# Optimization experiments

Hardware: AMD Instinct MI355X
Metric: run time of the kernel (lower is better)

Reference implementation:

```python
import jax, jax.numpy as jnp
import numpy as np

N_NODES = 200000
N_EDGES = 600000
EMB = 128
HID = 128
N_RELS = 64
N_MOTIFS = 512
N_CENTERS = 256
N_NODE_CLASSES = 16


def _linear_params(key, out_dim, in_dim):
    kw, kb = jax.random.split(key)
    s = 1.0 / np.sqrt(in_dim)
    w = jax.random.uniform(kw, (out_dim, in_dim), jnp.float32, -s, s)
    b = jax.random.uniform(kb, (out_dim,), jnp.float32, -s, s)
    return w, b


def setup_inputs() -> dict:
    key = jax.random.key(0)
    ks = jax.random.split(key, 12)
    lin_w, lin_b = _linear_params(ks[2], HID, EMB)
    conv1_w, conv1_b = _linear_params(ks[3], HID, HID)
    conv2_w, conv2_b = _linear_params(ks[4], HID, HID)
    edge_w, edge_b = _linear_params(ks[5], N_RELS, 2 * HID)
    motif_w, motif_b = _linear_params(ks[6], N_MOTIFS, HID)
    node_w, node_b = _linear_params(ks[7], N_NODE_CLASSES, HID)
    return {
        "node_emb": jax.random.normal(ks[0], (N_NODES, EMB), jnp.float32),
        "rel_emb": jax.random.normal(ks[1], (N_RELS, EMB), jnp.float32),
        "lin_w": lin_w, "lin_b": lin_b,
        "conv1_w": conv1_w, "conv1_b": conv1_b,
        "conv2_w": conv2_w, "conv2_b": conv2_b,
        "edge_w": edge_w, "edge_b": edge_b,
        "motif_w": motif_w, "motif_b": motif_b,
        "node_w": node_w, "node_b": node_b,
        "node_ids": jnp.arange(N_NODES, dtype=jnp.int32),
        "rel_ids": jax.random.randint(ks[8], (N_EDGES,), 0, N_RELS, jnp.int32),
        "center_mol_idx": jax.random.randint(ks[9], (N_CENTERS,), 0, N_NODES, jnp.int32),
        "edge_index": jax.random.randint(ks[10], (2, N_EDGES), 0, N_NODES, jnp.int32),
    }


def _gine_conv(x, edge_index, edge_attr, w, b):
    # PyG GINEConv (eps=0): nn((1+eps)*x + sum_j relu(x_j + e_ji))
    src, dst = edge_index[0], edge_index[1]
    msg = jax.nn.relu(x[src] + edge_attr)               # [E, H]
    agg = jax.ops.segment_sum(msg, dst, num_segments=x.shape[0])  # [N, H]
    return (agg + x) @ w.T + b


def reference(node_emb, rel_emb, lin_w, lin_b, conv1_w, conv1_b,
              conv2_w, conv2_b, edge_w, edge_b, motif_w, motif_b,
              node_w, node_b, node_ids, rel_ids, center_mol_idx, edge_index):
    x = node_emb[node_ids]            # [N, EMB]
    edge_attr = rel_emb[rel_ids]      # [E, EMB]
    x = x @ lin_w.T + lin_b           # [N, H]
    edge_attr = edge_attr @ lin_w.T + lin_b  # [E, H]
    x = _gine_conv(x, edge_index, edge_attr, conv1_w, conv1_b)
    x = jax.nn.relu(x)
    x = _gine_conv(x, edge_index, edge_attr, conv2_w, conv2_b)
    edge_pred_input = jnp.concatenate([x[edge_index[0]], x[edge_index[1]]], axis=1)  # [E, 2H]
    edge_class = edge_pred_input @ edge_w.T + edge_b       # [E, num_rels]
    center = x[center_mol_idx]                             # [C, H]
    motif_pred = center @ motif_w.T + motif_b              # [C, num_motifs]
    node_class = x @ node_w.T + node_b                     # [N, 16]
    return (edge_class, motif_pred, node_class)
```

## Files before the change

kernel.cpp:

```cpp
#include <hip/hip_runtime.h>
#include <hip/hip_bf16.h>

#define N_NODES 200000
#define N_EDGES 600000
#define EMB 128
#define HID 128
#define N_RELS 64
#define N_MOTIFS 512
#define N_CENTERS 256
#define NCLS 16

#define SCAN_C 512
#define NB_SCAN ((N_NODES + SCAN_C - 1) / SCAN_C)

typedef unsigned short u16;
typedef __attribute__((ext_vector_type(8))) short short8;
typedef __attribute__((ext_vector_type(4))) float f32x4;

__device__ __forceinline__ float bf2f(u16 u) {
    unsigned int i = ((unsigned int)u) << 16;
    float f; __builtin_memcpy(&f, &i, 4); return f;
}
__device__ __forceinline__ u16 f2bf(float f) {
    unsigned int x; __builtin_memcpy(&x, &f, 4);
    x += 0x7fffu + ((x >> 16) & 1u);
    return (u16)(x >> 16);
}

#define O_LINW   0
#define O_LINB   16384
#define O_C1W    16512
#define O_C1B    32896
#define O_C2W    33024
#define O_C2B    49408
#define O_EW     49536
#define O_EB     65920
#define O_MW     65984
#define O_MB     131520
#define O_NW     132032
#define O_NB     134080
#define N_WB     134096

__global__ void k_pre(const float* __restrict__ rel_emb,
                      const float* __restrict__ lw, const float* __restrict__ lb,
                      const float* __restrict__ c1w, const float* __restrict__ c1b,
                      const float* __restrict__ c2w, const float* __restrict__ c2b,
                      const float* __restrict__ ew, const float* __restrict__ eb,
                      const float* __restrict__ mw, const float* __restrict__ mb,
                      const float* __restrict__ nw, const float* __restrict__ nb,
                      float* __restrict__ rel_lin, u16* __restrict__ rel_bf,
                      u16* __restrict__ wb)
{
    if (blockIdx.x < 64) {
        __shared__ float e[EMB];
        const int r = blockIdx.x, h = threadIdx.x;
        e[h] = rel_emb[r * EMB + h];
        __syncthreads();
        const float* wr = lw + (size_t)h * EMB;
        float acc = lb[h];
        #pragma unroll
        for (int k0 = 0; k0 < EMB; k0 += 4) {
            f32x4 wv = *(const f32x4*)(wr + k0);
            #pragma unroll
            for (int j = 0; j < 4; ++j) acc += e[k0 + j] * wv[j];
        }
        rel_lin[r * HID + h] = acc;
        rel_bf[r * HID + h] = f2bf(acc);
        return;
    }
    const int t = (blockIdx.x - 64) * 128 + threadIdx.x;
    if (t >= N_WB) return;
    float v;
    if      (t < O_LINB) v = lw[t - O_LINW];
    else if (t < O_C1W)  v = lb[t - O_LINB];
    else if (t < O_C1B)  v = c1w[t - O_C1W];
    else if (t < O_C2W)  v = c1b[t - O_C1B];
    else if (t < O_C2B)  v = c2w[t - O_C2W];
    else if (t < O_EW)   v = c2b[t - O_C2B];
    else if (t < O_EB)   v = ew[t - O_EW];
    else if (t < O_MW)   v = eb[t - O_EB];
    else if (t < O_MB)   v = mw[t - O_MW];
    else if (t < O_NW)   v = mb[t - O_MB];
    else if (t < O_NB)   v = nw[t - O_NW];
    else                 v = nb[t - O_NB];
    wb[t] = f2bf(v);
}

__global__ void k_hist(const int* __restrict__ dst, int* __restrict__ deg)
{
    const int e = blockIdx.x * 256 + threadIdx.x;
    if (e < N_EDGES) atomicAdd(&deg[dst[e]], 1);
}

__global__ void k_scan1(const int* __restrict__ deg, int* __restrict__ bsum)
{
    __shared__ int sd[256];
    const int t = threadIdx.x, base = blockIdx.x * SCAN_C;
    int v = 0;
    int i0 = base + t, i1 = base + 256 + t;
    if (i0 < N_NODES) v += deg[i0];
    if (i1 < N_NODES) v += deg[i1];
    sd[t] = v; __syncthreads();
    for (int s = 128; s > 0; s >>= 1) {
        if (t < s) sd[t] += sd[t + s];
        __syncthreads();
    }
    if (t == 0) bsum[blockIdx.x] = sd[0];
}

__global__ void k_scan2(int* __restrict__ bsum, int* __restrict__ row_ptr)
{
    __shared__ int sh[512];
    const int t = threadIdx.x;
    int v = (t < NB_SCAN) ? bsum[t] : 0;
    sh[t] = v;
    for (int off = 1; off < 512; off <<= 1) {
        __syncthreads();
        int a = (t >= off) ? sh[t - off] : 0;
        __syncthreads();
        sh[t] += a;
    }
    __syncthreads();
    if (t < NB_SCAN) bsum[t] = sh[t] - v;
    if (t == 511) row_ptr[N_NODES] = sh[511];
}

__global__ void k_scan3(const int* __restrict__ deg, const int* __restrict__ bsum,
                        int* __restrict__ row_ptr)
{
    __shared__ int sh[256];
    const int t = threadIdx.x, base = blockIdx.x * SCAN_C;
    const int i0 = base + 2 * t, i1 = i0 + 1;
    int d0 = (i0 < N_NODES) ? deg[i0] : 0;
    int d1 = (i1 < N_NODES) ? deg[i1] : 0;
    int p = d0 + d1;
    sh[t] = p;
    for (int off = 1; off < 256; off <<= 1) {
        __syncthreads();
        int a = (t >= off) ? sh[t - off] : 0;
        __syncthreads();
        sh[t] += a;
    }
    __syncthreads();
    const int off = bsum[blockIdx.x] + sh[t] - p;
    if (i0 < N_NODES) row_ptr[i0] = off;
    if (i1 < N_NODES) row_ptr[i1] = off + d0;
}

__global__ void k_fill(const int* __restrict__ src, const int* __restrict__ dst,
                       const int* __restrict__ rid, const int* __restrict__ row_ptr,
                       int* __restrict__ cur, int* __restrict__ srcrid)
{
    const int e = blockIdx.x * 256 + threadIdx.x;
    if (e >= N_EDGES) return;
    const int d = dst[e];
    const int pos = row_ptr[d] + atomicAdd(&cur[d], 1);
    srcrid[pos] = src[e] * 64 + rid[e];
}

__global__ __launch_bounds__(256) void k_lin(
    const float* __restrict__ emb, const int* __restrict__ ids,
    const u16* __restrict__ w, const u16* __restrict__ bias,
    u16* __restrict__ out)
{
    const int wid = threadIdx.x >> 6, lane = threadIdx.x & 63;
    const int r15 = lane & 15, kg = (lane >> 4) * 8;
    const int arow = blockIdx.x * 64 + wid * 16 + r15;
    const int srow = ids[arow];
    const float* ar = emb + (size_t)srow * EMB + kg;
    short8 a[4];
    #pragma unroll
    for (int kk = 0; kk < 4; ++kk) {
        f32x4 a0 = *(const f32x4*)(ar + kk * 32);
        f32x4 a1 = *(const f32x4*)(ar + kk * 32 + 4);
        short8 t;
        #pragma unroll
        for (int j = 0; j < 4; ++j) { t[j] = (short)f2bf(a0[j]); t[4 + j] = (short)f2bf(a1[j]); }
        a[kk] = t;
    }
    f32x4 acc[8];
    #pragma unroll
    for (int nb = 0; nb < 8; ++nb) acc[nb] = (f32x4){0.f, 0.f, 0.f, 0.f};
    #pragma unroll
    for (int nb = 0; nb < 8; ++nb) {
        const u16* wr = w + (size_t)(nb * 16 + r15) * EMB + kg;
        #pragma unroll
        for (int kk = 0; kk < 4; ++kk) {
            short8 bv = *(const short8*)(wr + kk * 32);
            acc[nb] = __builtin_amdgcn_mfma_f32_16x16x32_bf16(a[kk], bv, acc[nb], 0, 0, 0);
        }
    }
    const int ob = blockIdx.x * 64 + wid * 16 + (lane >> 4) * 4;
    #pragma unroll
    for (int nb = 0; nb < 8; ++nb) {
        const int col = nb * 16 + r15;
        const float bn = bf2f(bias[col]);
        #pragma unroll
        for (int r = 0; r < 4; ++r)
            out[(size_t)(ob + r) * HID + col] = f2bf(acc[nb][r] + bn);
    }
}

__global__ __launch_bounds__(256) void k_msg2(
    const u16* __restrict__ x, const u16* __restrict__ relb,
    const int* __restrict__ srcrid, u16* __restrict__ msg)
{
    const int t = blockIdx.x * 256 + threadIdx.x;
    const int p = t >> 2;
    const int q = (t & 3) * 32;
    const int v = srcrid[p];
    const int s = v >> 6, r = v & 63;
    const u16* xp = x + (size_t)s * HID + q;
    const u16* rp = relb + r * HID + q;
    u16* mp = msg + (size_t)p * HID + q;
    #pragma unroll
    for (int c = 0; c < 4; ++c) {
        short8 xv = *(const short8*)(xp + c * 8);
        short8 rv = *(const short8*)(rp + c * 8);
        short8 o;
        #pragma unroll
        for (int j = 0; j < 8; ++j)
            o[j] = (short)f2bf(fmaxf(bf2f((u16)xv[j]) + bf2f((u16)rv[j]), 0.f));
        *(short8*)(mp + c * 8) = o;
    }
}

__global__ __launch_bounds__(256) void k_fuse2(
    const u16* __restrict__ x, const u16* __restrict__ msg,
    const int* __restrict__ row_ptr,
    const u16* __restrict__ w, const u16* __restrict__ bias,
    u16* __restrict__ out, const int do_relu)
{
    const int wid = threadIdx.x >> 6, lane = threadIdx.x & 63;
    const int r15 = lane & 15;
    const int kg = (lane >> 4) * 8;
    const int n = blockIdx.x * 64 + wid * 16 + r15;
    const int pbeg = row_ptr[n], pend = row_ptr[n + 1];

    float acc[32];
    #pragma unroll
    for (int j = 0; j < 32; ++j) acc[j] = 0.f;

    int p = pbeg;
    for (; p + 2 <= pend; p += 2) {
        const u16* m0 = msg + (size_t)p * HID + kg;
        const u16* m1 = m0 + HID;
        short8 v0[4], v1[4];
        #pragma unroll
        for (int kk = 0; kk < 4; ++kk) { v0[kk] = *(const short8*)(m0 + kk * 32);
                                         v1[kk] = *(const short8*)(m1 + kk * 32); }
        #pragma unroll
        for (int kk = 0; kk < 4; ++kk)
            #pragma unroll
            for (int j = 0; j < 8; ++j)
                acc[kk * 8 + j] += bf2f((u16)v0[kk][j]) + bf2f((u16)v1[kk][j]);
    }
    if (p < pend) {
        const u16* m0 = msg + (size_t)p * HID + kg;
        #pragma unroll
        for (int kk = 0; kk < 4; ++kk) {
            short8 v0 = *(const short8*)(m0 + kk * 32);
            #pragma unroll
            for (int j = 0; j < 8; ++j) acc[kk * 8 + j] += bf2f((u16)v0[j]);
        }
    }

    short8 a[4];
    {
        const u16* xp = x + (size_t)n * HID + kg;
        #pragma unroll
        for (int kk = 0; kk < 4; ++kk) {
            short8 xv = *(const short8*)(xp + kk * 32);
            short8 t;
            #pragma unroll
            for (int j = 0; j < 8; ++j) t[j] = (short)f2bf(acc[kk * 8 + j] + bf2f((u16)xv[j]));
            a[kk] = t;
        }
    }

    f32x4 accm[8];
    #pragma unroll
    for (int nb = 0; nb < 8; ++nb) accm[nb] = (f32x4){0.f, 0.f, 0.f, 0.f};
    #pragma unroll
    for (int nb = 0; nb < 8; ++nb) {
        const u16* wr = w + (size_t)(nb * 16 + r15) * HID + kg;
        #pragma unroll
        for (int kk = 0; kk < 4; ++kk) {
            short8 bv = *(const short8*)(wr + kk * 32);
            accm[nb] = __builtin_amdgcn_mfma_f32_16x16x32_bf16(a[kk], bv, accm[nb], 0, 0, 0);
        }
    }
    const int ob = blockIdx.x * 64 + wid * 16 + (lane >> 4) * 4;
    #pragma unroll
    for (int nb = 0; nb < 8; ++nb) {
        const int col = nb * 16 + r15;
        const float bn = bf2f(bias[col]);
        #pragma unroll
        for (int r = 0; r < 4; ++r) {
            float v = accm[nb][r] + bn;
            if (do_relu) v = fmaxf(v, 0.f);
            out[(size_t)(ob + r) * HID + col] = f2bf(v);
        }
    }
}

__global__ __launch_bounds__(256) void k_heads(
    const u16* __restrict__ x2, const u16* __restrict__ ew,
    const u16* __restrict__ nw, const u16* __restrict__ nbias,
    u16* __restrict__ y, float* __restrict__ node_out)
{
    const int wid = threadIdx.x >> 6, lane = threadIdx.x & 63;
    const int r15 = lane & 15, kg = (lane >> 4) * 8;
    const int arow = blockIdx.x * 64 + wid * 16 + r15;
    const u16* xr = x2 + (size_t)arow * HID + kg;
    short8 a[4];
    #pragma unroll
    for (int kk = 0; kk < 4; ++kk) a[kk] = *(const short8*)(xr + kk * 32);

    f32x4 accs[4], accd[4], accn;
    #pragma unroll
    for (int nb = 0; nb < 4; ++nb) {
        accs[nb] = (f32x4){0.f, 0.f, 0.f, 0.f};
        accd[nb] = (f32x4){0.f, 0.f, 0.f, 0.f};
    }
    accn = (f32x4){0.f, 0.f, 0.f, 0.f};

    #pragma unroll
    for (int nb = 0; nb < 4; ++nb) {
        const u16* wr = ew + (size_t)(nb * 16 + r15) * 256 + kg;
        #pragma unroll
        for (int kk = 0; kk < 4; ++kk) {
            short8 bs = *(const short8*)(wr + kk * 32);
            short8 bd = *(const short8*)(wr + 128 + kk * 32);
            accs[nb] = __builtin_amdgcn_mfma_f32_16x16x32_bf16(a[kk], bs, accs[nb], 0, 0, 0);
            accd[nb] = __builtin_amdgcn_mfma_f32_16x16x32_bf16(a[kk], bd, accd[nb], 0, 0, 0);
        }
    }
    {
        const u16* wr = nw + (size_t)r15 * HID + kg;
        #pragma unroll
        for (int kk = 0; kk < 4; ++kk) {
            short8 bv = *(const short8*)(wr + kk * 32);
            accn = __builtin_amdgcn_mfma_f32_16x16x32_bf16(a[kk], bv, accn, 0, 0, 0);
        }
    }

    const int ob = blockIdx.x * 64 + wid * 16 + (lane >> 4) * 4;
    #pragma unroll
    for (int nb = 0; nb < 4; ++nb) {
        const int col = nb * 16 + r15;
        #pragma unroll
        for (int r = 0; r < 4; ++r) {
            y[(size_t)(ob + r) * 128 + col] = f2bf(accs[nb][r]);
            y[(size_t)(ob + r) * 128 + 64 + col] = f2bf(accd[nb][r]);
        }
    }
    const float bn = bf2f(nbias[r15]);
    #pragma unroll
    for (int r = 0; r < 4; ++r)
        node_out[(size_t)(ob + r) * NCLS + r15] = accn[r] + bn;
}

__global__ __launch_bounds__(256) void k_eout(
    const u16* __restrict__ y, const int* __restrict__ src, const int* __restrict__ dst,
    const float* __restrict__ eb, float* __restrict__ out)
{
    const int t = blockIdx.x * 256 + threadIdx.x;
    const int e = t >> 2;
    const int qq = (t & 3) * 16;
    const int s = src[e], d = dst[e];
    const u16* ys = y + (size_t)s * 128 + qq;
    const u16* yd = y + (size_t)d * 128 + 64 + qq;
    const float* ebp = eb + qq;
    float* op = out + (size_t)e * 64 + qq;
    #pragma unroll
    for (int c = 0; c < 2; ++c) {
        short8 vs = *(const short8*)(ys + c * 8);
        short8 vd = *(const short8*)(yd + c * 8);
        #pragma unroll
        for (int h = 0; h < 2; ++h) {
            f32x4 vb = *(const f32x4*)(ebp + c * 8 + h * 4);
            f32x4 r;
            #pragma unroll
            for (int j = 0; j < 4; ++j)
                r[j] = bf2f((u16)vs[h * 4 + j]) + bf2f((u16)vd[h * 4 + j]) + vb[j];
            *(f32x4*)(op + c * 8 + h * 4) = r;
        }
    }
}

__global__ void k_motif(const u16* __restrict__ x2, const int* __restrict__ centers,
                        const u16* __restrict__ mw, const u16* __restrict__ mb,
                        float* __restrict__ out)
{
    __shared__ float xs[HID];
    const int c = blockIdx.x, m = threadIdx.x;
    if (m < HID) xs[m] = bf2f(x2[(size_t)centers[c] * HID + m]);
    __syncthreads();
    const u16* wr = mw + (size_t)m * HID;
    float acc = bf2f(mb[m]);
    #pragma unroll
    for (int k0 = 0; k0 < HID; k0 += 8) {
        short8 wv = *(const short8*)(wr + k0);
        #pragma unroll
        for (int j = 0; j < 8; ++j) acc += xs[k0 + j] * bf2f((u16)wv[j]);
    }
    out[(size_t)c * N_MOTIFS + m] = acc;
}

extern "C" void kernel_launch(void* const* d_in, const int* in_sizes, int n_in,
                              void* d_out, int out_size, void* d_ws, size_t ws_size,
                              hipStream_t stream)
{
    const float* node_emb = (const float*)d_in[0];
    const float* rel_emb  = (const float*)d_in[1];
    const float* lin_w    = (const float*)d_in[2];
    const float* lin_b    = (const float*)d_in[3];
    const float* conv1_w  = (const float*)d_in[4];
    const float* conv1_b  = (const float*)d_in[5];
    const float* conv2_w  = (const float*)d_in[6];
    const float* conv2_b  = (const float*)d_in[7];
    const float* edge_w   = (const float*)d_in[8];
    const float* edge_b   = (const float*)d_in[9];
    const float* motif_w  = (const float*)d_in[10];
    const float* motif_b  = (const float*)d_in[11];
    const float* node_w   = (const float*)d_in[12];
    const float* node_b   = (const float*)d_in[13];
    const int* node_ids = (const int*)d_in[14];
    const int* rel_ids  = (const int*)d_in[15];
    const int* centers  = (const int*)d_in[16];
    const int* src      = (const int*)d_in[17];
    const int* dst      = ((const int*)d_in[17]) + N_EDGES;

    char* ws = (char*)d_ws;
    float* rel_lin = (float*)ws;
    u16*   wb      = (u16*)(ws + 32768);
    u16*   rel_bf  = (u16*)(ws + 393216);
    u16*   x0      = (u16*)(ws + 524288);
    u16*   x1      = (u16*)(ws + 524288 + 51200000);
    u16*   y       = (u16*)(ws + 524288 + 2 * 51200000);
    char*  csr     = ws + 524288 + 3 * 51200000;
    int*   deg     = (int*)csr;
    int*   cur     = (int*)(csr + 800000);
    int*   row_ptr = (int*)(csr + 1600000);
    int*   srcrid  = (int*)(csr + 2400032);
    int*   bsum    = (int*)(csr + 4800032);
    u16*   x2      = x0;

    float* out_edge  = (float*)d_out;
    float* out_motif = out_edge + (size_t)N_EDGES * 64;
    float* out_node  = out_motif + (size_t)N_CENTERS * N_MOTIFS;

    u16* msg = (u16*)d_out;

    k_pre<<<64 + (N_WB + 127) / 128, 128, 0, stream>>>(
        rel_emb, lin_w, lin_b, conv1_w, conv1_b, conv2_w, conv2_b,
        edge_w, edge_b, motif_w, motif_b, node_w, node_b, rel_lin, rel_bf, wb);
    hipMemsetAsync(deg, 0, 1600000, stream);

    k_hist<<<(N_EDGES + 255) / 256, 256, 0, stream>>>(dst, deg);
    k_scan1<<<NB_SCAN, 256, 0, stream>>>(deg, bsum);
    k_scan2<<<1, 512, 0, stream>>>(bsum, row_ptr);
    k_scan3<<<NB_SCAN, 256, 0, stream>>>(deg, bsum, row_ptr);
    k_fill<<<(N_EDGES + 255) / 256, 256, 0, stream>>>(src, dst, rel_ids, row_ptr, cur, srcrid);

    k_lin<<<N_NODES / 64, 256, 0, stream>>>(node_emb, node_ids, wb + O_LINW, wb + O_LINB, x0);

    k_msg2<<<(N_EDGES * 4) / 256, 256, 0, stream>>>(x0, rel_bf, srcrid, msg);
    k_fuse2<<<N_NODES / 64, 256, 0, stream>>>(x0, msg, row_ptr,
                                              wb + O_C1W, wb + O_C1B, x1, 1);
    k_msg2<<<(N_EDGES * 4) / 256, 256, 0, stream>>>(x1, rel_bf, srcrid, msg);
    k_fuse2<<<N_NODES / 64, 256, 0, stream>>>(x1, msg, row_ptr,
                                              wb + O_C2W, wb + O_C2B, x2, 0);

    k_heads<<<N_NODES / 64, 256, 0, stream>>>(x2, wb + O_EW, wb + O_NW, wb + O_NB, y, out_node);
    k_eout<<<(N_EDGES * 4) / 256, 256, 0, stream>>>(y, src, dst, edge_b, out_edge);
    k_motif<<<N_CENTERS, N_MOTIFS, 0, stream>>>(x2, centers, wb + O_MW, wb + O_MB, out_motif);
}
```

Measured before the change: 558.4 us.

## Fuse message gather into GINE aggregation kernel, skipping materialized message buffer

Removes the separate message kernel that wrote relu(x[src]+rel) per edge to a scratch buffer. Each node's incoming edges are now gathered directly inside the aggregation kernel: 16 nodes per 128-thread block, each thread handling 16 channels. The summed row is staged through shared memory for the MFMA linear layer, and each wave computes 64 output columns. This saves a 600k x 128 bf16 write and read per layer and one launch, at the cost of scattered gathers from x and smaller blocks. Rounding also changes slightly, since messages are no longer rounded to bf16 before summation.

```diff
diff --git a/kernel.cpp b/kernel.cpp
--- a/kernel.cpp
+++ b/kernel.cpp
@@ -201,99 +201,100 @@
     }
 }
 
-__global__ __launch_bounds__(256) void k_msg2(
+#define ALD 136
+__global__ __launch_bounds__(128) void k_fuse(
     const u16* __restrict__ x, const u16* __restrict__ relb,
-    const int* __restrict__ srcrid, u16* __restrict__ msg)
-{
-    const int t = blockIdx.x * 256 + threadIdx.x;
-    const int p = t >> 2;
-    const int q = (t & 3) * 32;
-    const int v = srcrid[p];
-    const int s = v >> 6, r = v & 63;
-    const u16* xp = x + (size_t)s * HID + q;
-    const u16* rp = relb + r * HID + q;
-    u16* mp = msg + (size_t)p * HID + q;
-    #pragma unroll
-    for (int c = 0; c < 4; ++c) {
-        short8 xv = *(const short8*)(xp + c * 8);
-        short8 rv = *(const short8*)(rp + c * 8);
-        short8 o;
-        #pragma unroll
-        for (int j = 0; j < 8; ++j)
-            o[j] = (short)f2bf(fmaxf(bf2f((u16)xv[j]) + bf2f((u16)rv[j]), 0.f));
-        *(short8*)(mp + c * 8) = o;
-    }
-}
-
-__global__ __launch_bounds__(256) void k_fuse2(
-    const u16* __restrict__ x, const u16* __restrict__ msg,
-    const int* __restrict__ row_ptr,
+    const int* __restrict__ row_ptr, const int* __restrict__ srcrid,
     const u16* __restrict__ w, const u16* __restrict__ bias,
     u16* __restrict__ out, const int do_relu)
 {
-    const int wid = threadIdx.x >> 6, lane = threadIdx.x & 63;
-    const int r15 = lane & 15;
-    const int kg = (lane >> 4) * 8;
-    const int n = blockIdx.x * 64 + wid * 16 + r15;
+    __shared__ u16 atile[16 * ALD];
+
+    const int nl = threadIdx.x & 15;
+    const int g  = threadIdx.x >> 4;
+    const int ch = g * 16;
+    const int n = blockIdx.x * 16 + nl;
     const int pbeg = row_ptr[n], pend = row_ptr[n + 1];
 
-    float acc[32];
-    #pragma unroll
-    for (int j = 0; j < 32; ++j) acc[j] = 0.f;
+    float acc[16];
+    #pragma unroll
+    for (int j = 0; j < 16; ++j) acc[j] = 0.f;
 
     int p = pbeg;
     for (; p + 2 <= pend; p += 2) {
-        const u16* m0 = msg + (size_t)p * HID + kg;
-        const u16* m1 = m0 + HID;
-        short8 v0[4], v1[4];
-        #pragma unroll
-        for (int kk = 0; kk < 4; ++kk) { v0[kk] = *(const short8*)(m0 + kk * 32);
-                                         v1[kk] = *(const short8*)(m1 + kk * 32); }
-        #pragma unroll
-        for (int kk = 0; kk < 4; ++kk)
+        const int v0 = srcrid[p], v1 = srcrid[p + 1];
+        const int s0 = v0 >> 6, r0 = v0 & 63;
+        const int s1 = v1 >> 6, r1 = v1 & 63;
+        const u16* xp0 = x + (size_t)s0 * HID + ch;
+        const u16* xp1 = x + (size_t)s1 * HID + ch;
+        const u16* rp0 = relb + r0 * HID + ch;
+        const u16* rp1 = relb + r1 * HID + ch;
+        short8 xv0[2], xv1[2], rv0[2], rv1[2];
+        #pragma unroll
+        for (int c = 0; c < 2; ++c) {
+            xv0[c] = *(const short8*)(xp0 + c * 8);
+            xv1[c] = *(const short8*)(xp1 + c * 8);
+            rv0[c] = *(const short8*)(rp0 + c * 8);
+            rv1[c] = *(const short8*)(rp1 + c * 8);
+        }
+        #pragma unroll
+        for (int c = 0; c < 2; ++c)
+            #pragma unroll
+            for (int j = 0; j < 8; ++j) {
+                acc[c * 8 + j] += fmaxf(bf2f((u16)xv0[c][j]) + bf2f((u16)rv0[c][j]), 0.f);
+                acc[c * 8 + j] += fmaxf(bf2f((u16)xv1[c][j]) + bf2f((u16)rv1[c][j]), 0.f);
+            }
+    }
+    if (p < pend) {
+        const int v = srcrid[p];
+        const int s = v >> 6, r = v & 63;
+        const u16* xp = x + (size_t)s * HID + ch;
+        const u16* rp = relb + r * HID + ch;
+        #pragma unroll
+        for (int c = 0; c < 2; ++c) {
+            short8 xv = *(const short8*)(xp + c * 8);
+            short8 rv = *(const short8*)(rp + c * 8);
             #pragma unroll
             for (int j = 0; j < 8; ++j)
-                acc[kk * 8 + j] += bf2f((u16)v0[kk][j]) + bf2f((u16)v1[kk][j]);
-    }
-    if (p < pend) {
-        const u16* m0 = msg + (size_t)p * HID + kg;
-        #pragma unroll
-        for (int kk = 0; kk < 4; ++kk) {
-            short8 v0 = *(const short8*)(m0 + kk * 32);
-            #pragma unroll
-            for (int j = 0; j < 8; ++j) acc[kk * 8 + j] += bf2f((u16)v0[j]);
-        }
-    }
-
-    short8 a[4];
+                acc[c * 8 + j] += fmaxf(bf2f((u16)xv[j]) + bf2f((u16)rv[j]), 0.f);
+        }
+    }
     {
-        const u16* xp = x + (size_t)n * HID + kg;
-        #pragma unroll
-        for (int kk = 0; kk < 4; ++kk) {
-            short8 xv = *(const short8*)(xp + kk * 32);
+        const u16* xp = x + (size_t)n * HID + ch;
+        #pragma unroll
+        for (int c = 0; c < 2; ++c) {
+            short8 xv = *(const short8*)(xp + c * 8);
             short8 t;
             #pragma unroll
-            for (int j = 0; j < 8; ++j) t[j] = (short)f2bf(acc[kk * 8 + j] + bf2f((u16)xv[j]));
-            a[kk] = t;
-        }
-    }
-
-    f32x4 accm[8];
-    #pragma unroll
-    for (int nb = 0; nb < 8; ++nb) accm[nb] = (f32x4){0.f, 0.f, 0.f, 0.f};
-    #pragma unroll
-    for (int nb = 0; nb < 8; ++nb) {
-        const u16* wr = w + (size_t)(nb * 16 + r15) * HID + kg;
+            for (int j = 0; j < 8; ++j) t[j] = (short)f2bf(acc[c * 8 + j] + bf2f((u16)xv[j]));
+            *(short8*)(&atile[nl * ALD + ch + c * 8]) = t;
+        }
+    }
+    __syncthreads();
+
+    const int wid = threadIdx.x >> 6, lane = threadIdx.x & 63;
+    const int r15 = lane & 15, kg = (lane >> 4) * 8;
+    short8 a[4];
+    #pragma unroll
+    for (int kk = 0; kk < 4; ++kk)
+        a[kk] = *(const short8*)(&atile[r15 * ALD + kg + kk * 32]);
+
+    f32x4 accm[4];
+    #pragma unroll
+    for (int nb = 0; nb < 4; ++nb) accm[nb] = (f32x4){0.f, 0.f, 0.f, 0.f};
+    #pragma unroll
+    for (int nb = 0; nb < 4; ++nb) {
+        const u16* wr = w + (size_t)(wid * 64 + nb * 16 + r15) * HID + kg;
         #pragma unroll
         for (int kk = 0; kk < 4; ++kk) {
             short8 bv = *(const short8*)(wr + kk * 32);
             accm[nb] = __builtin_amdgcn_mfma_f32_16x16x32_bf16(a[kk], bv, accm[nb], 0, 0, 0);
         }
     }
-    const int ob = blockIdx.x * 64 + wid * 16 + (lane >> 4) * 4;
-    #pragma unroll
-    for (int nb = 0; nb < 8; ++nb) {
-        const int col = nb * 16 + r15;
+    const int ob = blockIdx.x * 16 + (lane >> 4) * 4;
+    #pragma unroll
+    for (int nb = 0; nb < 4; ++nb) {
+        const int col = wid * 64 + nb * 16 + r15;
         const float bn = bf2f(bias[col]);
         #pragma unroll
         for (int r = 0; r < 4; ++r) {
@@ -451,8 +452,6 @@
     float* out_motif = out_edge + (size_t)N_EDGES * 64;
     float* out_node  = out_motif + (size_t)N_CENTERS * N_MOTIFS;
 
-    u16* msg = (u16*)d_out;
-
     k_pre<<<64 + (N_WB + 127) / 128, 128, 0, stream>>>(
         rel_emb, lin_w, lin_b, conv1_w, conv1_b, conv2_w, conv2_b,
         edge_w, edge_b, motif_w, motif_b, node_w, node_b, rel_lin, rel_bf, wb);
@@ -466,12 +465,10 @@
 
     k_lin<<<N_NODES / 64, 256, 0, stream>>>(node_emb, node_ids, wb + O_LINW, wb + O_LINB, x0);
 
-    k_msg2<<<(N_EDGES * 4) / 256, 256, 0, stream>>>(x0, rel_bf, srcrid, msg);
-    k_fuse2<<<N_NODES / 64, 256, 0, stream>>>(x0, msg, row_ptr,
-                                              wb + O_C1W, wb + O_C1B, x1, 1);
-    k_msg2<<<(N_EDGES * 4) / 256, 256, 0, stream>>>(x1, rel_bf, srcrid, msg);
-    k_fuse2<<<N_NODES / 64, 256, 0, stream>>>(x1, msg, row_ptr,
-                                              wb + O_C2W, wb + O_C2B, x2, 0);
+    k_fuse<<<N_NODES / 16, 128, 0, stream>>>(x0, rel_bf, row_ptr, srcrid,
+                                             wb + O_C1W, wb + O_C1B, x1, 1);
+    k_fuse<<<N_NODES / 16, 128, 0, stream>>>(x1, rel_bf, row_ptr, srcrid,
+                                             wb + O_C2W, wb + O_C2B, x2, 0);
 
     k_heads<<<N_NODES / 64, 256, 0, stream>>>(x2, wb + O_EW, wb + O_NW, wb + O_NB, y, out_node);
     k_eout<<<(N_EDGES * 4) / 256, 256, 0, stream>>>(y, src, dst, edge_b, out_edge);
```

Measured after the change: 497.8 us. 1.12x faster.
